# Performance work log

Hardware: AMD Instinct MI355X
Metric: run time of the kernel (lower is better)

Reference implementation:

```python
import jax, jax.numpy as jnp
import numpy as np

B, N = 8, 48
NEMBED, EMBED_DIM, HID_DIM = 1000, 32, 32
IN_DIM = EMBED_DIM + 1  # feature dim after concatenating xfeat
N_OPS = 8  # exchangeable 3-tensor basis: identity + means over each nonempty axis subset


def setup_inputs() -> dict:
    key = jax.random.key(0)
    k1, k2, k3, k4, k5 = jax.random.split(key, 5)
    xcat = jax.random.randint(k1, (B, N), 0, NEMBED)
    xfeat = jax.random.normal(k2, (B, N), dtype=jnp.float32)
    embed_table = jax.random.normal(k3, (NEMBED, EMBED_DIM), dtype=jnp.float32)
    # SetEq3to3 coefficients: (in_dim, n_basis_ops, out_dim), Glorot-ish scale
    coefs = jax.random.normal(k4, (IN_DIM, N_OPS, HID_DIM), dtype=jnp.float32) * np.sqrt(2.0 / (IN_DIM + HID_DIM))
    eq_bias = jnp.zeros((HID_DIM,), dtype=jnp.float32)
    out_w = jax.random.normal(k5, (HID_DIM, 1), dtype=jnp.float32) * np.sqrt(1.0 / HID_DIM)
    out_b = jnp.zeros((1,), dtype=jnp.float32)
    return {"xcat": xcat, "xfeat": xfeat, "embed_table": embed_table,
            "coefs": coefs, "eq_bias": eq_bias, "out_w": out_w, "out_b": out_b}


def _set_eq3to3(t, coefs, eq_bias):
    # t: (B, d, n, n, n); coefs: (d, 8, h). Each basis op is a mean over a
    # subset of the three set axes (kept as size-1 dims so broadcasting restores shape).
    def mix(op, s):
        return jnp.einsum('bd...,dh->bh...', op, coefs[:, s, :])
    m_i = t.mean(axis=2, keepdims=True)
    m_j = t.mean(axis=3, keepdims=True)
    m_k = t.mean(axis=4, keepdims=True)
    m_ij = m_i.mean(axis=3, keepdims=True)
    m_ik = m_i.mean(axis=4, keepdims=True)
    m_jk = m_j.mean(axis=4, keepdims=True)
    m_ijk = m_ij.mean(axis=4, keepdims=True)
    out = (mix(t, 0) + mix(m_i, 1) + mix(m_j, 2) + mix(m_k, 3)
           + mix(m_ij, 4) + mix(m_ik, 5) + mix(m_jk, 6) + mix(m_ijk, 7))
    return out + eq_bias.reshape(1, -1, 1, 1, 1)  # (B, h, n, n, n)


def reference(xcat, xfeat, embed_table, coefs, eq_bias, out_w, out_b):
    e = embed_table[xcat]                                   # (B, n, d_e)
    x = jnp.concatenate([e, xfeat[..., None]], axis=-1)      # (B, n, d) with d = d_e + 1
    t = jnp.einsum('bid,bjd,bkd->bdijk', x, x, x)            # (B, d, n, n, n)
    y = _set_eq3to3(t, coefs, eq_bias)                       # (B, h, n, n, n)
    y = jnp.transpose(y, (0, 2, 3, 4, 1))                    # (B, n, n, n, h)
    y = jax.nn.relu(y)
    y = y.mean(axis=(1, 2, 3))                               # (B, h) mean pool
    y = jax.nn.relu(y)
    # dropout is inactive in eval mode (training=False)
    return y @ out_w + out_b                                 # (B, 1)
```

## Files before the change

### kernel.cpp

```cpp
#include <hip/hip_runtime.h>
#include <cstdint>
#include <cstddef>

#define BB 8
#define NN 48
#define DD 33
#define XS 40
#define KP 128
#define HH 32
#define MM (NN*NN)
#define NC (NN*HH)
#define TILE 96
#define TM (MM/TILE)
#define TN (NC/TILE)
#define NBLK (TM*TN)
#define LDK 136

typedef __attribute__((ext_vector_type(8))) _Float16 f16x8;
typedef __attribute__((ext_vector_type(4))) float f32x4;

__global__ void k_setup(const int* __restrict__ xcat, const float* __restrict__ xfeat,
                        const float* __restrict__ embed, const float* __restrict__ coefs,
                        float* __restrict__ xw, float* __restrict__ sw,
                        float* __restrict__ ct) {
    int b = blockIdx.x, t = threadIdx.x;
    if (b < BB) {
        for (int idx = t; idx < NN * XS; idx += 256) {
            int i = idx / XS, d = idx - i * XS;
            float v = 0.f;
            if (d < 32)       v = embed[xcat[b * NN + i] * 32 + d];
            else if (d == 32) v = xfeat[b * NN + i];
            xw[b * NN * XS + idx] = v;
        }
        __syncthreads();
        if (t < XS) {
            float a = 0.f;
            for (int i = 0; i < NN; ++i) a += xw[b * NN * XS + i * XS + t];
            sw[b * XS + t] = a * (1.0f / 48.0f);
        }
    } else {
        for (int idx = t; idx < 8 * HH * XS; idx += 256) {
            int qh = idx / XS, d = idx - qh * XS;
            int q = qh >> 5, h = qh & 31;
            ct[idx] = (d < DD) ? coefs[(d * 8 + q) * HH + h] : 0.f;
        }
    }
}

__global__ void k_buildD(const float* __restrict__ xw, const float* __restrict__ sw,
                         const float* __restrict__ ct, const float* __restrict__ eq_bias,
                         _Float16* __restrict__ Dw) {
    int idx = blockIdx.x * 256 + threadIdx.x;
    int rowid = idx >> 4, d0 = (idx & 15) * 8;
    int b = rowid / NC, n = rowid - b * NC;
    int k = n >> 5, h = n & 31;
    const float* xk = xw + (b * NN + k) * XS;
    const float* sb = sw + b * XS;
    f16x8 v;
    if (d0 < 120) {
        int seg = (d0 >= 80) ? 2 : (d0 >= 40) ? 1 : 0;
        int d = d0 - seg * 40;
        const int QA[3] = {0, 2, 1}, QB[3] = {3, 6, 5};
        const float* ca = ct + (QA[seg] * HH + h) * XS + d;
        const float* cb = ct + (QB[seg] * HH + h) * XS + d;
        f32x4 ca0 = *(const f32x4*)(ca),     ca1 = *(const f32x4*)(ca + 4);
        f32x4 cb0 = *(const f32x4*)(cb),     cb1 = *(const f32x4*)(cb + 4);
        f32x4 xk0 = *(const f32x4*)(xk + d), xk1 = *(const f32x4*)(xk + d + 4);
        f32x4 sb0 = *(const f32x4*)(sb + d), sb1 = *(const f32x4*)(sb + d + 4);
        f32x4 r0 = ca0 * xk0 + cb0 * sb0;
        f32x4 r1 = ca1 * xk1 + cb1 * sb1;
        for (int e = 0; e < 4; ++e) { v[e] = (_Float16)r0[e]; v[4 + e] = (_Float16)r1[e]; }
    } else {
        const float* c4 = ct + (4 * HH + h) * XS;
        const float* c7 = ct + (7 * HH + h) * XS;
        float g = 0.f;
        for (int d = 0; d < DD; ++d) {
            float sd = sb[d];
            g += sd * sd * (c4[d] * xk[d] + c7[d] * sd);
        }
        v = (f16x8){0, 0, 0, 0, 0, 0, 0, 0};
        v[0] = (_Float16)(g + eq_bias[h]);
    }
    *(f16x8*)&Dw[(size_t)rowid * KP + d0] = v;
}

__global__ __launch_bounds__(256) void k_gemm(const float* __restrict__ xw,
                                              const float* __restrict__ sw,
                                              const _Float16* __restrict__ Dw,
                                              float* __restrict__ partials) {
    __shared__ __align__(16) _Float16 As[TILE][LDK];
    __shared__ __align__(16) _Float16 Bs[TILE][LDK];
    __shared__ float hacc[HH];
    int t = threadIdx.x;
    int bx = blockIdx.x, by = blockIdx.y, b = blockIdx.z;
    int M0 = by * TILE, N0 = bx * TILE;
    if (t < HH) hacc[t] = 0.f;

    const _Float16* Dg = Dw + ((size_t)(b * NC + N0)) * KP;
    const float* xb = xw + b * NN * XS;
    const float* sb = sw + b * XS;

    for (int c = 0; c < 6; ++c) {
        int ch = c * 256 + t;
        int row = ch >> 4, d0 = (ch & 15) * 8;
        *(f16x8*)&Bs[row][d0] = *(const f16x8*)(Dg + row * KP + d0);
        int grow = M0 + row;
        int i = grow / NN, j = grow - i * NN;
        f16x8 v;
        if (d0 < 120) {
            int seg = (d0 >= 80) ? 2 : (d0 >= 40) ? 1 : 0;
            int d = d0 - seg * 40;
            const float* p1 = (seg == 2) ? (xb + j * XS) : (xb + i * XS);
            const float* p2 = (seg == 0) ? (xb + j * XS) : sb;
            f32x4 a0 = *(const f32x4*)(p1 + d), a1 = *(const f32x4*)(p1 + d + 4);
            f32x4 b0 = *(const f32x4*)(p2 + d), b1 = *(const f32x4*)(p2 + d + 4);
            f32x4 r0 = a0 * b0, r1 = a1 * b1;
            for (int e = 0; e < 4; ++e) { v[e] = (_Float16)r0[e]; v[4 + e] = (_Float16)r1[e]; }
        } else {
            v = (f16x8){0, 0, 0, 0, 0, 0, 0, 0};
            v[0] = (_Float16)1.f;
        }
        *(f16x8*)&As[row][d0] = v;
    }
    __syncthreads();

    int lane = t & 63, wave = t >> 6;
    int wm = (wave >> 1) * 48, wn = (wave & 1) * 48;
    int lrow = lane & 15, quad = lane >> 4;

    f32x4 acc[3][3];
    for (int mt = 0; mt < 3; ++mt)
        for (int nt = 0; nt < 3; ++nt)
            acc[mt][nt] = (f32x4){0.f, 0.f, 0.f, 0.f};

    for (int ks = 0; ks < 4; ++ks) {
        f16x8 af[3], bf[3];
        for (int mt = 0; mt < 3; ++mt)
            af[mt] = *(const f16x8*)&As[wm + mt * 16 + lrow][ks * 32 + quad * 8];
        for (int nt = 0; nt < 3; ++nt)
            bf[nt] = *(const f16x8*)&Bs[wn + nt * 16 + lrow][ks * 32 + quad * 8];
        for (int mt = 0; mt < 3; ++mt)
            for (int nt = 0; nt < 3; ++nt)
                acc[mt][nt] = __builtin_amdgcn_mfma_f32_16x16x32_f16(af[mt], bf[nt], acc[mt][nt], 0, 0, 0);
    }

    float fs[3] = {0.f, 0.f, 0.f};
    for (int mt = 0; mt < 3; ++mt)
        for (int nt = 0; nt < 3; ++nt)
            for (int r = 0; r < 4; ++r)
                fs[nt] += fmaxf(acc[mt][nt][r], 0.f);
    for (int nt = 0; nt < 3; ++nt) {
        int h = (N0 + wn + nt * 16 + lrow) & 31;
        atomicAdd(&hacc[h], fs[nt]);
    }
    __syncthreads();
    if (t < HH) {
        int blockLin = by * TN + bx;
        partials[((size_t)b * NBLK + blockLin) * HH + t] = hacc[t];
    }
}

__global__ void k_final(const float* __restrict__ partials, const float* __restrict__ out_w,
                        const float* __restrict__ out_b, float* __restrict__ out) {
    __shared__ float red[256];
    int b = blockIdx.x, t = threadIdx.x;
    int h = t & 31, g = t >> 5;
    float a = 0.f;
    for (int p = g; p < NBLK; p += 8) a += partials[((size_t)b * NBLK + p) * HH + h];
    red[t] = a;
    __syncthreads();
    if (t < HH) {
        float tot = 0.f;
        for (int gg = 0; gg < 8; ++gg) tot += red[gg * 32 + t];
        float m = tot * (1.0f / 110592.0f);
        red[t] = fmaxf(m, 0.f) * out_w[t];
    }
    __syncthreads();
    if (t == 0) {
        float o = 0.f;
        for (int h2 = 0; h2 < HH; ++h2) o += red[h2];
        out[b] = o + out_b[0];
    }
}

extern "C" void kernel_launch(void* const* d_in, const int* in_sizes, int n_in,
                              void* d_out, int out_size, void* d_ws, size_t ws_size,
                              hipStream_t stream) {
    (void)in_sizes; (void)n_in; (void)out_size; (void)ws_size;
    const int*   xcat    = (const int*)d_in[0];
    const float* xfeat   = (const float*)d_in[1];
    const float* embed   = (const float*)d_in[2];
    const float* coefs   = (const float*)d_in[3];
    const float* eq_bias = (const float*)d_in[4];
    const float* out_w   = (const float*)d_in[5];
    const float* out_b   = (const float*)d_in[6];
    float* out = (float*)d_out;

    char* w = (char*)d_ws;
    float*    xw       = (float*)(w + 0);
    float*    sw       = (float*)(w + 61440);
    float*    ct       = (float*)(w + 62720);
    _Float16* Dw       = (_Float16*)(w + 103680);
    float*    partials = (float*)(w + 3249408);

    k_setup<<<dim3(BB + 1), dim3(256), 0, stream>>>(xcat, xfeat, embed, coefs, xw, sw, ct);
    k_buildD<<<dim3(768), dim3(256), 0, stream>>>(xw, sw, ct, eq_bias, Dw);
    k_gemm<<<dim3(TN, TM, BB), dim3(256), 0, stream>>>(xw, sw, Dw, partials);
    k_final<<<dim3(BB), dim3(256), 0, stream>>>(partials, out_w, out_b, out);
}
```

Before: 127.3 us.

## Fuse D-matrix build and final reduction into GEMM, loop over M tiles per block

Removes the separate buildD kernel and the global Dw buffer by building the B tile in shared memory inside the GEMM block. Each block now keeps its B tile and fragments in registers while looping over several M tiles, which amortises the B construction. The final pooled reduction is folded into the GEMM through global atomics and a last-block-done counter, which removes the k_final launch. In exchange there are fewer blocks (less parallelism), the A build is serialized with the MFMA work, and float atomics make the summation order nondeterministic.

```diff
diff --git a/kernel.cpp b/kernel.cpp
--- a/kernel.cpp
+++ b/kernel.cpp
@@ -13,7 +13,9 @@
 #define TILE 96
 #define TM (MM/TILE)
 #define TN (NC/TILE)
-#define NBLK (TM*TN)
+#define SPLITM 4
+#define MQ (TM/SPLITM)
+#define NBLK (TN*SPLITM*BB)
 #define LDK 136
 
 typedef __attribute__((ext_vector_type(8))) _Float16 f16x8;
@@ -22,7 +24,8 @@
 __global__ void k_setup(const int* __restrict__ xcat, const float* __restrict__ xfeat,
                         const float* __restrict__ embed, const float* __restrict__ coefs,
                         float* __restrict__ xw, float* __restrict__ sw,
-                        float* __restrict__ ct) {
+                        float* __restrict__ ct, float* __restrict__ hacc_g,
+                        unsigned int* __restrict__ counter) {
     int b = blockIdx.x, t = threadIdx.x;
     if (b < BB) {
         for (int idx = t; idx < NN * XS; idx += 256) {
@@ -38,39 +41,40 @@
             for (int i = 0; i < NN; ++i) a += xw[b * NN * XS + i * XS + t];
             sw[b * XS + t] = a * (1.0f / 48.0f);
         }
-    } else {
+    } else if (b == BB) {
         for (int idx = t; idx < 8 * HH * XS; idx += 256) {
             int qh = idx / XS, d = idx - qh * XS;
             int q = qh >> 5, h = qh & 31;
             ct[idx] = (d < DD) ? coefs[(d * 8 + q) * HH + h] : 0.f;
         }
+    } else {
+        if (t < BB * HH) hacc_g[t] = 0.f;
+        if (t == 0) *counter = 0u;
     }
 }
 
-__global__ void k_buildD(const float* __restrict__ xw, const float* __restrict__ sw,
-                         const float* __restrict__ ct, const float* __restrict__ eq_bias,
-                         _Float16* __restrict__ Dw) {
-    int idx = blockIdx.x * 256 + threadIdx.x;
-    int rowid = idx >> 4, d0 = (idx & 15) * 8;
-    int b = rowid / NC, n = rowid - b * NC;
-    int k = n >> 5, h = n & 31;
-    const float* xk = xw + (b * NN + k) * XS;
+__global__ __launch_bounds__(256, 2) void k_gemm(
+        const float* __restrict__ xw, const float* __restrict__ sw,
+        const float* __restrict__ ct, const float* __restrict__ eq_bias,
+        float* __restrict__ hacc_g, unsigned int* __restrict__ counter,
+        const float* __restrict__ out_w, const float* __restrict__ out_b,
+        float* __restrict__ out) {
+    __shared__ __align__(16) _Float16 As[TILE][LDK];
+    __shared__ __align__(16) _Float16 Bs[TILE][LDK];
+    __shared__ float gbuf[TILE];
+    __shared__ float hacc[HH];
+    __shared__ int lastFlag;
+
+    int t = threadIdx.x;
+    int bx = blockIdx.x, my = blockIdx.y, b = blockIdx.z;
+    int N0 = bx * TILE;
+    const float* xb = xw + b * NN * XS;
     const float* sb = sw + b * XS;
-    f16x8 v;
-    if (d0 < 120) {
-        int seg = (d0 >= 80) ? 2 : (d0 >= 40) ? 1 : 0;
-        int d = d0 - seg * 40;
-        const int QA[3] = {0, 2, 1}, QB[3] = {3, 6, 5};
-        const float* ca = ct + (QA[seg] * HH + h) * XS + d;
-        const float* cb = ct + (QB[seg] * HH + h) * XS + d;
-        f32x4 ca0 = *(const f32x4*)(ca),     ca1 = *(const f32x4*)(ca + 4);
-        f32x4 cb0 = *(const f32x4*)(cb),     cb1 = *(const f32x4*)(cb + 4);
-        f32x4 xk0 = *(const f32x4*)(xk + d), xk1 = *(const f32x4*)(xk + d + 4);
-        f32x4 sb0 = *(const f32x4*)(sb + d), sb1 = *(const f32x4*)(sb + d + 4);
-        f32x4 r0 = ca0 * xk0 + cb0 * sb0;
-        f32x4 r1 = ca1 * xk1 + cb1 * sb1;
-        for (int e = 0; e < 4; ++e) { v[e] = (_Float16)r0[e]; v[4 + e] = (_Float16)r1[e]; }
-    } else {
+
+    if (t < HH) hacc[t] = 0.f;
+    if (t < TILE) {
+        int n = N0 + t, k = n >> 5, h = n & 31;
+        const float* xk = xb + k * XS;
         const float* c4 = ct + (4 * HH + h) * XS;
         const float* c7 = ct + (7 * HH + h) * XS;
         float g = 0.f;
@@ -78,108 +82,140 @@
             float sd = sb[d];
             g += sd * sd * (c4[d] * xk[d] + c7[d] * sd);
         }
-        v = (f16x8){0, 0, 0, 0, 0, 0, 0, 0};
-        v[0] = (_Float16)(g + eq_bias[h]);
-    }
-    *(f16x8*)&Dw[(size_t)rowid * KP + d0] = v;
-}
-
-__global__ __launch_bounds__(256) void k_gemm(const float* __restrict__ xw,
-                                              const float* __restrict__ sw,
-                                              const _Float16* __restrict__ Dw,
-                                              float* __restrict__ partials) {
-    __shared__ __align__(16) _Float16 As[TILE][LDK];
-    __shared__ __align__(16) _Float16 Bs[TILE][LDK];
-    __shared__ float hacc[HH];
-    int t = threadIdx.x;
-    int bx = blockIdx.x, by = blockIdx.y, b = blockIdx.z;
-    int M0 = by * TILE, N0 = bx * TILE;
-    if (t < HH) hacc[t] = 0.f;
-
-    const _Float16* Dg = Dw + ((size_t)(b * NC + N0)) * KP;
-    const float* xb = xw + b * NN * XS;
-    const float* sb = sw + b * XS;
+        gbuf[t] = g + eq_bias[h];
+    }
+    __syncthreads();
 
     for (int c = 0; c < 6; ++c) {
         int ch = c * 256 + t;
         int row = ch >> 4, d0 = (ch & 15) * 8;
-        *(f16x8*)&Bs[row][d0] = *(const f16x8*)(Dg + row * KP + d0);
-        int grow = M0 + row;
-        int i = grow / NN, j = grow - i * NN;
+        int n = N0 + row, k = n >> 5, h = n & 31;
+        const float* xk = xb + k * XS;
         f16x8 v;
         if (d0 < 120) {
             int seg = (d0 >= 80) ? 2 : (d0 >= 40) ? 1 : 0;
             int d = d0 - seg * 40;
-            const float* p1 = (seg == 2) ? (xb + j * XS) : (xb + i * XS);
-            const float* p2 = (seg == 0) ? (xb + j * XS) : sb;
-            f32x4 a0 = *(const f32x4*)(p1 + d), a1 = *(const f32x4*)(p1 + d + 4);
-            f32x4 b0 = *(const f32x4*)(p2 + d), b1 = *(const f32x4*)(p2 + d + 4);
-            f32x4 r0 = a0 * b0, r1 = a1 * b1;
+            const int QA[3] = {0, 2, 1}, QB[3] = {3, 6, 5};
+            const float* ca = ct + (QA[seg] * HH + h) * XS + d;
+            const float* cb = ct + (QB[seg] * HH + h) * XS + d;
+            f32x4 ca0 = *(const f32x4*)(ca),     ca1 = *(const f32x4*)(ca + 4);
+            f32x4 cb0 = *(const f32x4*)(cb),     cb1 = *(const f32x4*)(cb + 4);
+            f32x4 xk0 = *(const f32x4*)(xk + d), xk1 = *(const f32x4*)(xk + d + 4);
+            f32x4 sb0 = *(const f32x4*)(sb + d), sb1 = *(const f32x4*)(sb + d + 4);
+            f32x4 r0 = ca0 * xk0 + cb0 * sb0;
+            f32x4 r1 = ca1 * xk1 + cb1 * sb1;
             for (int e = 0; e < 4; ++e) { v[e] = (_Float16)r0[e]; v[4 + e] = (_Float16)r1[e]; }
         } else {
             v = (f16x8){0, 0, 0, 0, 0, 0, 0, 0};
-            v[0] = (_Float16)1.f;
-        }
-        *(f16x8*)&As[row][d0] = v;
-    }
+            v[0] = (_Float16)gbuf[row];
+        }
+        *(f16x8*)&Bs[row][d0] = v;
+    }
+
+    auto buildA = [&](int mt) {
+        int M0 = (my * MQ + mt) * TILE;
+        for (int c = 0; c < 6; ++c) {
+            int ch = c * 256 + t;
+            int row = ch >> 4, d0 = (ch & 15) * 8;
+            int grow = M0 + row;
+            int i = grow / NN, j = grow - i * NN;
+            f16x8 v;
+            if (d0 < 120) {
+                int seg = (d0 >= 80) ? 2 : (d0 >= 40) ? 1 : 0;
+                int d = d0 - seg * 40;
+                const float* p1 = (seg == 2) ? (xb + j * XS) : (xb + i * XS);
+                const float* p2 = (seg == 0) ? (xb + j * XS) : sb;
+                f32x4 a0 = *(const f32x4*)(p1 + d), a1 = *(const f32x4*)(p1 + d + 4);
+                f32x4 b0 = *(const f32x4*)(p2 + d), b1 = *(const f32x4*)(p2 + d + 4);
+                f32x4 r0 = a0 * b0, r1 = a1 * b1;
+                for (int e = 0; e < 4; ++e) { v[e] = (_Float16)r0[e]; v[4 + e] = (_Float16)r1[e]; }
+            } else {
+                v = (f16x8){0, 0, 0, 0, 0, 0, 0, 0};
+                v[0] = (_Float16)1.f;
+            }
+            *(f16x8*)&As[row][d0] = v;
+        }
+    };
+
+    buildA(0);
     __syncthreads();
 
     int lane = t & 63, wave = t >> 6;
     int wm = (wave >> 1) * 48, wn = (wave & 1) * 48;
     int lrow = lane & 15, quad = lane >> 4;
 
-    f32x4 acc[3][3];
-    for (int mt = 0; mt < 3; ++mt)
-        for (int nt = 0; nt < 3; ++nt)
-            acc[mt][nt] = (f32x4){0.f, 0.f, 0.f, 0.f};
-
-    for (int ks = 0; ks < 4; ++ks) {
-        f16x8 af[3], bf[3];
-        for (int mt = 0; mt < 3; ++mt)
-            af[mt] = *(const f16x8*)&As[wm + mt * 16 + lrow][ks * 32 + quad * 8];
-        for (int nt = 0; nt < 3; ++nt)
-            bf[nt] = *(const f16x8*)&Bs[wn + nt * 16 + lrow][ks * 32 + quad * 8];
-        for (int mt = 0; mt < 3; ++mt)
+    f16x8 bf[3][4];
+#pragma unroll
+    for (int nt = 0; nt < 3; ++nt)
+#pragma unroll
+        for (int ks = 0; ks < 4; ++ks)
+            bf[nt][ks] = *(const f16x8*)&Bs[wn + nt * 16 + lrow][ks * 32 + quad * 8];
+
+    float fs[3] = {0.f, 0.f, 0.f};
+    for (int mt = 0; mt < MQ; ++mt) {
+        f32x4 acc[3][3];
+#pragma unroll
+        for (int m3 = 0; m3 < 3; ++m3)
+#pragma unroll
             for (int nt = 0; nt < 3; ++nt)
-                acc[mt][nt] = __builtin_amdgcn_mfma_f32_16x16x32_f16(af[mt], bf[nt], acc[mt][nt], 0, 0, 0);
-    }
-
-    float fs[3] = {0.f, 0.f, 0.f};
-    for (int mt = 0; mt < 3; ++mt)
-        for (int nt = 0; nt < 3; ++nt)
-            for (int r = 0; r < 4; ++r)
-                fs[nt] += fmaxf(acc[mt][nt][r], 0.f);
+                acc[m3][nt] = (f32x4){0.f, 0.f, 0.f, 0.f};
+
+#pragma unroll
+        for (int ks = 0; ks < 4; ++ks) {
+            f16x8 af[3];
+#pragma unroll
+            for (int m3 = 0; m3 < 3; ++m3)
+                af[m3] = *(const f16x8*)&As[wm + m3 * 16 + lrow][ks * 32 + quad * 8];
+#pragma unroll
+            for (int m3 = 0; m3 < 3; ++m3)
+#pragma unroll
+                for (int nt = 0; nt < 3; ++nt)
+                    acc[m3][nt] = __builtin_amdgcn_mfma_f32_16x16x32_f16(af[m3], bf[nt][ks], acc[m3][nt], 0, 0, 0);
+        }
+
+#pragma unroll
+        for (int m3 = 0; m3 < 3; ++m3)
+#pragma unroll
+            for (int nt = 0; nt < 3; ++nt)
+#pragma unroll
+                for (int r = 0; r < 4; ++r)
+                    fs[nt] += fmaxf(acc[m3][nt][r], 0.f);
+
+        __syncthreads();
+        if (mt + 1 < MQ) {
+            buildA(mt + 1);
+            __syncthreads();
+        }
+    }
+
+#pragma unroll
     for (int nt = 0; nt < 3; ++nt) {
-        int h = (N0 + wn + nt * 16 + lrow) & 31;
-        atomicAdd(&hacc[h], fs[nt]);
-    }
-    __syncthreads();
-    if (t < HH) {
-        int blockLin = by * TN + bx;
-        partials[((size_t)b * NBLK + blockLin) * HH + t] = hacc[t];
-    }
-}
-
-__global__ void k_final(const float* __restrict__ partials, const float* __restrict__ out_w,
-                        const float* __restrict__ out_b, float* __restrict__ out) {
-    __shared__ float red[256];
-    int b = blockIdx.x, t = threadIdx.x;
-    int h = t & 31, g = t >> 5;
-    float a = 0.f;
-    for (int p = g; p < NBLK; p += 8) a += partials[((size_t)b * NBLK + p) * HH + h];
-    red[t] = a;
-    __syncthreads();
-    if (t < HH) {
-        float tot = 0.f;
-        for (int gg = 0; gg < 8; ++gg) tot += red[gg * 32 + t];
-        float m = tot * (1.0f / 110592.0f);
-        red[t] = fmaxf(m, 0.f) * out_w[t];
-    }
+        float v = fs[nt];
+        v += __shfl_xor(v, 16);
+        v += __shfl_xor(v, 32);
+        if (lane < 16) atomicAdd(&hacc[(wn + nt * 16 + lane) & 31], v);
+    }
+    __syncthreads();
+    if (t < HH) atomicAdd(&hacc_g[b * HH + t], hacc[t]);
+    __threadfence();
     __syncthreads();
     if (t == 0) {
-        float o = 0.f;
-        for (int h2 = 0; h2 < HH; ++h2) o += red[h2];
-        out[b] = o + out_b[0];
+        unsigned int tk = atomicAdd(counter, 1u);
+        lastFlag = (tk == NBLK - 1) ? 1 : 0;
+    }
+    __syncthreads();
+
+    if (lastFlag) {
+        int bb = t >> 5, h2 = t & 31;
+        float v = atomicAdd(&hacc_g[bb * HH + h2], 0.f);
+        float m = v * (1.0f / 110592.0f);
+        float r = fmaxf(m, 0.f) * out_w[h2];
+        r += __shfl_xor(r, 1);
+        r += __shfl_xor(r, 2);
+        r += __shfl_xor(r, 4);
+        r += __shfl_xor(r, 8);
+        r += __shfl_xor(r, 16);
+        if (h2 == 0) out[bb] = r + out_b[0];
     }
 }
 
@@ -197,14 +233,15 @@
     float* out = (float*)d_out;
 
     char* w = (char*)d_ws;
-    float*    xw       = (float*)(w + 0);
-    float*    sw       = (float*)(w + 61440);
-    float*    ct       = (float*)(w + 62720);
-    _Float16* Dw       = (_Float16*)(w + 103680);
-    float*    partials = (float*)(w + 3249408);
-
-    k_setup<<<dim3(BB + 1), dim3(256), 0, stream>>>(xcat, xfeat, embed, coefs, xw, sw, ct);
-    k_buildD<<<dim3(768), dim3(256), 0, stream>>>(xw, sw, ct, eq_bias, Dw);
-    k_gemm<<<dim3(TN, TM, BB), dim3(256), 0, stream>>>(xw, sw, Dw, partials);
-    k_final<<<dim3(BB), dim3(256), 0, stream>>>(partials, out_w, out_b, out);
+    float*        xw      = (float*)(w + 0);
+    float*        sw      = (float*)(w + 61440);
+    float*        ct      = (float*)(w + 62720);
+    float*        hacc_g  = (float*)(w + 103680);
+    unsigned int* counter = (unsigned int*)(w + 104704);
+
+    k_setup<<<dim3(BB + 2), dim3(256), 0, stream>>>(xcat, xfeat, embed, coefs,
+                                                    xw, sw, ct, hacc_g, counter);
+    k_gemm<<<dim3(TN, SPLITM, BB), dim3(256), 0, stream>>>(xw, sw, ct, eq_bias,
+                                                           hacc_g, counter,
+                                                           out_w, out_b, out);
 }
```

Result: no change. 126.4 us (-0.7%).
